# Optimization experiments

Hardware: AMD Instinct MI355X
Metric: run time of the kernel (lower is better)

The kernel has to match this reference:

```python
import jax, jax.numpy as jnp
import numpy as np

G, T, M, S = 16384, 200, 2, 8  # groups, timesteps, measures, state dim


def setup_inputs() -> dict:
    key = jax.random.key(0)
    ks = jax.random.split(key, 7)
    x = jax.random.normal(ks[0], (G, T, M), jnp.float32)
    m0 = jax.random.normal(ks[1], (G, S), jnp.float32)
    # per-group PSD initial covariance
    A = 0.1 * jax.random.normal(ks[2], (G, S, S), jnp.float32)
    P0 = jnp.einsum('gij,gkj->gik', A, A) + jnp.eye(S, dtype=jnp.float32)
    # near-identity stable transition matrix
    F = jnp.eye(S, dtype=jnp.float32) + 0.01 * jax.random.normal(ks[3], (S, S), jnp.float32)
    Bq = 0.1 * jax.random.normal(ks[4], (S, S), jnp.float32)
    Q = Bq @ Bq.T + 0.01 * jnp.eye(S, dtype=jnp.float32)
    H = jax.random.normal(ks[5], (M, S), jnp.float32) / np.float32(np.sqrt(S))
    Br = 0.1 * jax.random.normal(ks[6], (M, M), jnp.float32)
    R = Br @ Br.T + 0.1 * jnp.eye(M, dtype=jnp.float32)
    return {"x": x, "m0": m0, "P0": P0, "F": F, "Q": Q, "H": H, "R": R}


def reference(x, m0, P0, F, Q, H, R):
    """Batched Kalman filter producing one-step-ahead measurement predictions.

    x:  [G,T,M] observations. m0:[G,S], P0:[G,S,S]. F,Q:[S,S]. H:[M,S]. R:[M,M].
    Returns (meas_means [G,T,M], meas_covs [G,T,M,M]).
    Per the torch loop: at step t output measurement of the current prediction
    (H m, H P H^T + R), then update with x[:, t] and predict forward (F, Q).
    """
    def step(carry, x_t):
        m, P = carry                                   # [G,S], [G,S,S]
        HP = jnp.einsum('ms,gsk->gmk', H, P)           # [G,M,S]
        S_mat = jnp.einsum('gmk,nk->gmn', HP, H) + R   # innovation cov [G,M,M]
        meas_mean = m @ H.T                            # [G,M]
        # measurement update (Kalman gain K = P H^T S^{-1}; Kt = K^T = S^{-1} H P)
        y = x_t - meas_mean
        Kt = jnp.linalg.solve(S_mat, HP)               # [G,M,S]
        m_u = m + jnp.einsum('gms,gm->gs', Kt, y)
        P_u = P - jnp.einsum('gms,gmk->gsk', Kt, HP)   # (I - K H) P
        # time update
        m_p = m_u @ F.T
        P_p = jnp.einsum('ij,gjk,lk->gil', F, P_u, F) + Q
        return (m_p, P_p), (meas_mean, S_mat)

    (_, _), (means, covs) = jax.lax.scan(step, (m0, P0), jnp.swapaxes(x, 0, 1))
    return jnp.swapaxes(means, 0, 1), jnp.swapaxes(covs, 0, 1)
```

## Files before the change

kernel.cpp:

```cpp
#include <hip/hip_runtime.h>

#define NG 16384
#define NT 200

#define DPPF(v, ctrl) __int_as_float(__builtin_amdgcn_update_dpp( \
    0, __float_as_int(v), (ctrl), 0xF, 0xF, true))
#define QP1(v) DPPF(v, 0xB1)
#define QP2(v) DPPF(v, 0x4E)
#define RHM(v) DPPF(v, 0x141)
#define SWZ(v, e) __int_as_float(__builtin_amdgcn_ds_swizzle( \
    __float_as_int(v), ((e) << 10) | 0x1F))
#define PIN(v) asm volatile("" : "+v"(v))

__device__ __forceinline__ void gather8(float v, float* __restrict__ o) {
  o[0] = v;
  o[1] = QP1(v);
  o[2] = QP2(v);
  o[3] = QP2(o[1]);
  o[7] = RHM(v);
  o[6] = RHM(o[1]);
  o[5] = RHM(o[2]);
  o[4] = RHM(o[3]);
}
__device__ __forceinline__ void gatherS(float v, float* __restrict__ o) {
  o[0] = v;
  o[1] = SWZ(v, 1); o[2] = SWZ(v, 2); o[3] = SWZ(v, 3); o[4] = SWZ(v, 4);
  o[5] = SWZ(v, 5); o[6] = SWZ(v, 6); o[7] = SWZ(v, 7);
}

__global__ __launch_bounds__(256, 1)
void kf_kernel(const float* __restrict__ x,
               const float* __restrict__ m0,
               const float* __restrict__ P0,
               const float* __restrict__ Fm,
               const float* __restrict__ Qm,
               const float* __restrict__ Hm,
               const float* __restrict__ Rm,
               float* __restrict__ out) {
  const int tid = threadIdx.x;
  const int r   = tid & 7;
  const int g   = blockIdx.x * 32 + (tid >> 3);

  float Frt[8], Qt[8], Hd0[8], Hd1[8];
#pragma unroll
  for (int c = 0; c < 8; ++c) {
    Frt[c] = Fm[(r << 3) | (r ^ c)];
    Qt[c]  = Qm[(r << 3) | (r ^ c)];
    Hd0[c] = Hm[r ^ c];
    Hd1[c] = Hm[8 + (r ^ c)];
  }
  const float R00 = Rm[0], R01 = Rm[1], R11 = Rm[3];

  float Fde[8][8];
  {
    float t1[8], t2[8], t3[8], tt[8];
#pragma unroll
    for (int c = 0; c < 8; ++c) Fde[0][c] = Frt[c];
#pragma unroll
    for (int c = 0; c < 8; ++c) t1[c] = QP1(Frt[c]);
#pragma unroll
    for (int c = 0; c < 8; ++c) Fde[1][c] = t1[1 ^ c];
#pragma unroll
    for (int c = 0; c < 8; ++c) t2[c] = QP2(Frt[c]);
#pragma unroll
    for (int c = 0; c < 8; ++c) Fde[2][c] = t2[2 ^ c];
#pragma unroll
    for (int c = 0; c < 8; ++c) t3[c] = QP2(t1[c]);
#pragma unroll
    for (int c = 0; c < 8; ++c) Fde[3][c] = t3[3 ^ c];
#pragma unroll
    for (int c = 0; c < 8; ++c) tt[c] = RHM(Frt[c]);
#pragma unroll
    for (int c = 0; c < 8; ++c) Fde[7][c] = tt[7 ^ c];
#pragma unroll
    for (int c = 0; c < 8; ++c) tt[c] = RHM(t1[c]);
#pragma unroll
    for (int c = 0; c < 8; ++c) Fde[6][c] = tt[6 ^ c];
#pragma unroll
    for (int c = 0; c < 8; ++c) tt[c] = RHM(t2[c]);
#pragma unroll
    for (int c = 0; c < 8; ++c) Fde[5][c] = tt[5 ^ c];
#pragma unroll
    for (int c = 0; c < 8; ++c) tt[c] = RHM(t3[c]);
#pragma unroll
    for (int c = 0; c < 8; ++c) Fde[4][c] = tt[4 ^ c];
  }

  float HFd0[8], HFd1[8];
  {
    float Hs0[8], Hs1[8];
#pragma unroll
    for (int i = 0; i < 8; ++i) { Hs0[i] = Hm[i]; Hs1[i] = Hm[8 + i]; }
    float hfc0 = 0.f, hfc1 = 0.f;
#pragma unroll
    for (int jj = 0; jj < 8; ++jj) {
      const float fc = Fm[(jj << 3) | r];
      hfc0 = fmaf(Hs0[jj], fc, hfc0);
      hfc1 = fmaf(Hs1[jj], fc, hfc1);
    }
    gather8(hfc0, HFd0);
    gather8(hfc1, HFd1);
  }

#pragma unroll
  for (int e = 0; e < 8; ++e)
#pragma unroll
    for (int c = 0; c < 8; ++c) PIN(Fde[e][c]);
#pragma unroll
  for (int c = 0; c < 8; ++c) {
    PIN(Frt[c]); PIN(Qt[c]); PIN(Hd0[c]); PIN(Hd1[c]);
    PIN(HFd0[c]); PIN(HFd1[c]);
  }

  float m = m0[(size_t)g * 8 + r];
  float P[8];
#pragma unroll
  for (int d = 0; d < 8; ++d)
    P[d] = P0[(size_t)g * 64 + (r << 3) + (r ^ d)];

  const float* xg = x + (size_t)g * NT * 2;
  float* mo = out + (size_t)g * NT * 2;
  float* co = out + (size_t)NG * NT * 2 + (size_t)g * NT * 4;

  float mm0, mm1;
  {
    float MU[8];
    gather8(m, MU);
    float a = Hd0[0] * MU[0], b = Hd1[0] * MU[0];
#pragma unroll
    for (int e = 1; e < 8; ++e) {
      a = fmaf(Hd0[e], MU[e], a);
      b = fmaf(Hd1[e], MU[e], b);
    }
    mm0 = a; mm1 = b;
  }

  float4 xa = *reinterpret_cast<const float4*>(xg);
  float4 xb = *reinterpret_cast<const float4*>(xg + 4);
  float4 na = *reinterpret_cast<const float4*>(xg + 8);
  float4 nb = *reinterpret_cast<const float4*>(xg + 12);

#pragma unroll 1
  for (int tb = 0; tb < NT; tb += 4) {
#pragma unroll
    for (int j = 0; j < 4; ++j) {
      const int t = tb + j;
      const float x0 = (j == 0) ? xa.x : (j == 1) ? xa.z : (j == 2) ? xb.x : xb.z;
      const float x1 = (j == 0) ? xa.y : (j == 1) ? xa.w : (j == 2) ? xb.y : xb.w;

      float hp0 = Hd0[0] * P[0];
      float hp1 = Hd1[0] * P[0];
#pragma unroll
      for (int c = 1; c < 8; ++c) {
        hp0 = fmaf(Hd0[c], P[c], hp0);
        hp1 = fmaf(Hd1[c], P[c], hp1);
      }

      float G0[8], G1[8];
      gatherS(hp0, G0);
      gatherS(hp1, G1);

      if (r == 0) *reinterpret_cast<float2*>(mo + 2 * t) = make_float2(mm0, mm1);
      const float y0 = x0 - mm0, y1 = x1 - mm1;

      float sa = G0[0] * Hd0[0], sb = G0[0] * Hd1[0], sc = G1[0] * Hd1[0];
#pragma unroll
      for (int e = 1; e < 8; ++e) {
        sa = fmaf(G0[e], Hd0[e], sa);
        sb = fmaf(G0[e], Hd1[e], sb);
        sc = fmaf(G1[e], Hd1[e], sc);
      }
      const float s00 = R00 + sa, s01 = R01 + sb, s11 = R11 + sc;

      const float det  = fmaf(s00, s11, -(s01 * s01));
      const float rdet = 1.0f / det;
      const float kt0 = fmaf(s11, hp0, -(s01 * hp1)) * rdet;
      const float kt1 = fmaf(s00, hp1, -(s01 * hp0)) * rdet;

      const float mu = fmaf(kt0, y0, fmaf(kt1, y1, m));
      float MU[8];
      gatherS(mu, MU);

      if (r == 1) *reinterpret_cast<float4*>(co + 4 * t) = make_float4(s00, s01, s01, s11);

      float Pu[8];
#pragma unroll
      for (int d = 0; d < 8; ++d)
        Pu[d] = fmaf(-kt0, G0[d], fmaf(-kt1, G1[d], P[d]));

      float Ct[8];
#pragma unroll
      for (int e = 0; e < 8; ++e) {
        float acc = Fde[e][0] * Pu[0];
#pragma unroll
        for (int d = 1; d < 8; ++d) acc = fmaf(Fde[e][d], Pu[d], acc);
        Ct[e] = acc;
      }

      float Crow[8];
      Crow[0] = Ct[0];
      Crow[1] = SWZ(Ct[1], 1); Crow[2] = SWZ(Ct[2], 2);
      Crow[3] = SWZ(Ct[3], 3); Crow[4] = SWZ(Ct[4], 4);
      Crow[5] = SWZ(Ct[5], 5); Crow[6] = SWZ(Ct[6], 6);
      Crow[7] = SWZ(Ct[7], 7);

#pragma unroll
      for (int d = 0; d < 8; ++d) {
        float acc = fmaf(Fde[d][0], Crow[0], Qt[d]);
#pragma unroll
        for (int e = 1; e < 8; ++e) acc = fmaf(Fde[d][e], Crow[e], acc);
        P[d] = acc;
      }

      float ma = Frt[0] * MU[0], h0 = HFd0[0] * MU[0], h1 = HFd1[0] * MU[0];
#pragma unroll
      for (int e = 1; e < 8; ++e) {
        ma = fmaf(Frt[e],  MU[e], ma);
        h0 = fmaf(HFd0[e], MU[e], h0);
        h1 = fmaf(HFd1[e], MU[e], h1);
      }
      m = ma; mm0 = h0; mm1 = h1;
    }
    xa = na; xb = nb;
    int tf = tb + 8; if (tf > NT - 4) tf = NT - 4;
    na = *reinterpret_cast<const float4*>(xg + 2 * tf);
    nb = *reinterpret_cast<const float4*>(xg + 2 * tf + 4);
  }
}

extern "C" void kernel_launch(void* const* d_in, const int* in_sizes, int n_in,
                              void* d_out, int out_size, void* d_ws, size_t ws_size,
                              hipStream_t stream) {
  const float* x  = (const float*)d_in[0];
  const float* m0 = (const float*)d_in[1];
  const float* P0 = (const float*)d_in[2];
  const float* F  = (const float*)d_in[3];
  const float* Q  = (const float*)d_in[4];
  const float* H  = (const float*)d_in[5];
  const float* R  = (const float*)d_in[6];
  float* out = (float*)d_out;

  dim3 grid(NG * 8 / 256), block(256);
  hipLaunchKernelGGL(kf_kernel, grid, block, 0, stream,
                     x, m0, P0, F, Q, H, R, out);
}
```

Before: 160.7 us.

## Move F diagonal table to shared memory to cut registers and double occupancy

Drops the 64-register per-thread Fde table and the PIN register pins, and instead reads F rows in XOR-diagonal layout from a 64-float LDS array with float4 loads inside the covariance propagation. Launch bounds go from 1 to 2 blocks per SIMD so more waves can hide the latency of the long dependent chains. The cost is 16 extra LDS reads per timestep per thread and a block-wide sync before the loop.

```diff
diff --git a/kernel.cpp b/kernel.cpp
--- a/kernel.cpp
+++ b/kernel.cpp
@@ -10,7 +10,6 @@
 #define RHM(v) DPPF(v, 0x141)
 #define SWZ(v, e) __int_as_float(__builtin_amdgcn_ds_swizzle( \
     __float_as_int(v), ((e) << 10) | 0x1F))
-#define PIN(v) asm volatile("" : "+v"(v))
 
 __device__ __forceinline__ void gather8(float v, float* __restrict__ o) {
   o[0] = v;
@@ -28,7 +27,7 @@
   o[5] = SWZ(v, 5); o[6] = SWZ(v, 6); o[7] = SWZ(v, 7);
 }
 
-__global__ __launch_bounds__(256, 1)
+__global__ __launch_bounds__(256, 2)
 void kf_kernel(const float* __restrict__ x,
                const float* __restrict__ m0,
                const float* __restrict__ P0,
@@ -41,6 +40,12 @@
   const int r   = tid & 7;
   const int g   = blockIdx.x * 32 + (tid >> 3);
 
+  __shared__ float FxS[64];
+  if (tid < 64) {
+    const int i = tid >> 3, d = tid & 7;
+    FxS[(i << 3) | d] = Fm[(i << 3) | (i ^ d)];
+  }
+
   float Frt[8], Qt[8], Hd0[8], Hd1[8];
 #pragma unroll
   for (int c = 0; c < 8; ++c) {
@@ -50,41 +55,6 @@
     Hd1[c] = Hm[8 + (r ^ c)];
   }
   const float R00 = Rm[0], R01 = Rm[1], R11 = Rm[3];
-
-  float Fde[8][8];
-  {
-    float t1[8], t2[8], t3[8], tt[8];
-#pragma unroll
-    for (int c = 0; c < 8; ++c) Fde[0][c] = Frt[c];
-#pragma unroll
-    for (int c = 0; c < 8; ++c) t1[c] = QP1(Frt[c]);
-#pragma unroll
-    for (int c = 0; c < 8; ++c) Fde[1][c] = t1[1 ^ c];
-#pragma unroll
-    for (int c = 0; c < 8; ++c) t2[c] = QP2(Frt[c]);
-#pragma unroll
-    for (int c = 0; c < 8; ++c) Fde[2][c] = t2[2 ^ c];
-#pragma unroll
-    for (int c = 0; c < 8; ++c) t3[c] = QP2(t1[c]);
-#pragma unroll
-    for (int c = 0; c < 8; ++c) Fde[3][c] = t3[3 ^ c];
-#pragma unroll
-    for (int c = 0; c < 8; ++c) tt[c] = RHM(Frt[c]);
-#pragma unroll
-    for (int c = 0; c < 8; ++c) Fde[7][c] = tt[7 ^ c];
-#pragma unroll
-    for (int c = 0; c < 8; ++c) tt[c] = RHM(t1[c]);
-#pragma unroll
-    for (int c = 0; c < 8; ++c) Fde[6][c] = tt[6 ^ c];
-#pragma unroll
-    for (int c = 0; c < 8; ++c) tt[c] = RHM(t2[c]);
-#pragma unroll
-    for (int c = 0; c < 8; ++c) Fde[5][c] = tt[5 ^ c];
-#pragma unroll
-    for (int c = 0; c < 8; ++c) tt[c] = RHM(t3[c]);
-#pragma unroll
-    for (int c = 0; c < 8; ++c) Fde[4][c] = tt[4 ^ c];
-  }
 
   float HFd0[8], HFd1[8];
   {
@@ -102,16 +72,6 @@
     gather8(hfc1, HFd1);
   }
 
-#pragma unroll
-  for (int e = 0; e < 8; ++e)
-#pragma unroll
-    for (int c = 0; c < 8; ++c) PIN(Fde[e][c]);
-#pragma unroll
-  for (int c = 0; c < 8; ++c) {
-    PIN(Frt[c]); PIN(Qt[c]); PIN(Hd0[c]); PIN(Hd1[c]);
-    PIN(HFd0[c]); PIN(HFd1[c]);
-  }
-
   float m = m0[(size_t)g * 8 + r];
   float P[8];
 #pragma unroll
@@ -140,6 +100,8 @@
   float4 na = *reinterpret_cast<const float4*>(xg + 8);
   float4 nb = *reinterpret_cast<const float4*>(xg + 12);
 
+  __syncthreads();
+
 #pragma unroll 1
   for (int tb = 0; tb < NT; tb += 4) {
 #pragma unroll
@@ -191,9 +153,12 @@
       float Ct[8];
 #pragma unroll
       for (int e = 0; e < 8; ++e) {
-        float acc = Fde[e][0] * Pu[0];
-#pragma unroll
-        for (int d = 1; d < 8; ++d) acc = fmaf(Fde[e][d], Pu[d], acc);
+        const float4 fa = *reinterpret_cast<const float4*>(&FxS[((r ^ e) << 3)]);
+        const float4 fb = *reinterpret_cast<const float4*>(&FxS[((r ^ e) << 3) | 4]);
+        const float f8[8] = {fa.x, fa.y, fa.z, fa.w, fb.x, fb.y, fb.z, fb.w};
+        float acc = f8[e ^ 0] * Pu[0];
+#pragma unroll
+        for (int d = 1; d < 8; ++d) acc = fmaf(f8[e ^ d], Pu[d], acc);
         Ct[e] = acc;
       }
 
@@ -206,9 +171,12 @@
 
 #pragma unroll
       for (int d = 0; d < 8; ++d) {
-        float acc = fmaf(Fde[d][0], Crow[0], Qt[d]);
-#pragma unroll
-        for (int e = 1; e < 8; ++e) acc = fmaf(Fde[d][e], Crow[e], acc);
+        const float4 fa = *reinterpret_cast<const float4*>(&FxS[((r ^ d) << 3)]);
+        const float4 fb = *reinterpret_cast<const float4*>(&FxS[((r ^ d) << 3) | 4]);
+        const float f8[8] = {fa.x, fa.y, fa.z, fa.w, fb.x, fb.y, fb.z, fb.w};
+        float acc = fmaf(f8[d ^ 0], Crow[0], Qt[d]);
+#pragma unroll
+        for (int e = 1; e < 8; ++e) acc = fmaf(f8[d ^ e], Crow[e], acc);
         P[d] = acc;
       }
 
```

After: 200.8 us. 1.25x slower.
